# Optimization experiments

Measured on AMD Instinct MI355X. Metric: run time of the kernel, lower is better.

## Reference

```python
import jax, jax.numpy as jnp
import numpy as np

N_NODES = 100000  # size_u + size_v + size_w
N_MP = 3          # metapaths vv, uu, ww
N_EDGES = 1000000
D_IN = 64
D_OUT = 64


def setup_inputs() -> dict:
    key = jax.random.key(0)
    k1, k2, k3, k4 = jax.random.split(key, 4)
    x = jax.random.normal(k1, (N_NODES, D_IN), dtype=jnp.float32)
    # per-metapath GCNConv weight (glorot-ish scale)
    W = jax.random.normal(k2, (N_MP, D_IN, D_OUT), dtype=jnp.float32) * (1.0 / np.sqrt(D_IN))
    edge_index = jax.random.randint(k3, (N_MP, 2, N_EDGES), 0, N_NODES, dtype=jnp.int64)
    edge_weight = jax.random.uniform(k4, (N_MP, N_EDGES), dtype=jnp.float32)
    return {"x": x, "W": W, "edge_index": edge_index, "edge_weight": edge_weight}


def _gcn_conv(x, w_mat, row, col, ew, num_nodes):
    # gcn_norm without self-loops: deg[i] = sum of edge weights into i
    deg = jax.ops.segment_sum(ew, col, num_segments=num_nodes)
    dinv = jnp.where(deg > 0, jax.lax.rsqrt(jnp.where(deg > 0, deg, 1.0)), 0.0)
    norm = dinv[row] * ew * dinv[col]          # [E]
    h = x @ w_mat                               # [N, D_OUT]
    msg = h[row] * norm[:, None]                # [E, D_OUT] gather + scale
    return jax.ops.segment_sum(msg, col, num_segments=num_nodes)  # scatter-add


def reference(x, W, edge_index, edge_weight):
    num_nodes = x.shape[0]
    outs = []
    for i in range(N_MP):  # small fixed loop over structurally distinct encoders
        row = edge_index[i, 0]
        col = edge_index[i, 1]
        out = _gcn_conv(x, W[i], row, col, edge_weight[i], num_nodes)
        outs.append(jax.nn.relu(out))  # act=nn.ReLU
    return jnp.stack(outs)  # [3, N, D_OUT]; dropout omitted (eval mode)
```

## Files before the change

kernel.cpp:

```cpp
#include <hip/hip_runtime.h>

#define NNODES 100000
#define NMP 3
#define NEDGES 1000000
#define D 64
#define NTOT (NMP * NNODES)
#define BINW 1024
#define NBIN 293
#define CAPB 10944
#define T1 3072
#define OVCAP 131072

typedef __attribute__((ext_vector_type(8))) short bf16x8;
typedef __attribute__((ext_vector_type(4))) float floatx4;

__device__ __forceinline__ unsigned short f2bf(float f) {
    unsigned u = __float_as_uint(f);
    u = (u + 0x7FFFu + ((u >> 16) & 1u)) >> 16;
    return (unsigned short)u;
}
__device__ __forceinline__ float bf2f_lo(unsigned u) { return __uint_as_float(u << 16); }
__device__ __forceinline__ float bf2f_hi(unsigned u) { return __uint_as_float(u & 0xFFFF0000u); }

__global__ __launch_bounds__(512) void split_kernel(const int* __restrict__ ei,
                                                    const float* __restrict__ ew,
                                                    int* __restrict__ gcur,
                                                    int* __restrict__ ovcur,
                                                    int* __restrict__ ovf,
                                                    uint2* __restrict__ A) {
    __shared__ int hist[NBIN], binstart[NBIN], cur[NBIN], gb[NBIN];
    __shared__ int sA[512], sB[512];
    __shared__ uint2 tile[T1];
    __shared__ unsigned short tbin[T1];
    __shared__ int stotal;
    const int t = threadIdx.x;
    const int mp = blockIdx.y;
    const int e0 = blockIdx.x * T1;
    for (int i = t; i < NBIN; i += 512) { hist[i] = 0; cur[i] = 0; }
    __syncthreads();
    unsigned key[6]; float w[6]; int bn[6];
#pragma unroll
    for (int i = 0; i < 6; ++i) {
        int e = e0 + i * 512 + t;
        bn[i] = -1;
        if (e < NEDGES) {
            int r = ei[(mp * 2 + 0) * NEDGES + e];
            int c = ei[(mp * 2 + 1) * NEDGES + e];
            w[i] = ew[mp * NEDGES + e];
            int cflat = mp * NNODES + c;
            int rflat = mp * NNODES + r;
            int b = cflat >> 10;
            bn[i] = b;
            key[i] = ((unsigned)(cflat & 1023) << 19) | (unsigned)rflat;
            atomicAdd(&hist[b], 1);
        }
    }
    __syncthreads();
    int v = (t < NBIN) ? hist[t] : 0;
    sA[t] = v;
    __syncthreads();
    int* src = sA; int* dst = sB;
    for (int d = 1; d < 512; d <<= 1) {
        dst[t] = src[t] + ((t >= d) ? src[t - d] : 0);
        __syncthreads();
        int* tmp = src; src = dst; dst = tmp;
    }
    if (t < NBIN) {
        binstart[t] = src[t] - v;
        gb[t] = v ? atomicAdd(&gcur[t], v) : 0;
    }
    if (t == 511) stotal = src[511];
    __syncthreads();
#pragma unroll
    for (int i = 0; i < 6; ++i) {
        if (bn[i] >= 0) {
            int rk = atomicAdd(&cur[bn[i]], 1);
            int s = binstart[bn[i]] + rk;
            tile[s] = make_uint2(key[i], __float_as_uint(w[i]));
            tbin[s] = (unsigned short)bn[i];
        }
    }
    __syncthreads();
    int tot = stotal;
    for (int s = t; s < tot; s += 512) {
        uint2 rec = tile[s];
        int b = tbin[s];
        int pos = gb[b] + (s - binstart[b]);
        if (pos < CAPB) {
            A[(size_t)b * CAPB + pos] = rec;
        } else {
            int op = atomicAdd(ovcur, 1);
            if (op < OVCAP) {
                int cflat = (b << 10) | (int)(rec.x >> 19);
                ovf[3 * op] = cflat;
                ovf[3 * op + 1] = (int)(rec.x & 0x7FFFFu);
                ovf[3 * op + 2] = (int)rec.y;
            }
        }
    }
}

__global__ __launch_bounds__(256) void compact2_kernel(const int* __restrict__ gcur,
                                                       const uint2* __restrict__ A,
                                                       const int* __restrict__ ovcur,
                                                       const int* __restrict__ ovf,
                                                       uint2* __restrict__ C,
                                                       int2* __restrict__ nodeoff,
                                                       float* __restrict__ dinv) {
    const int bin = blockIdx.x;
    __shared__ int cnt[BINW];
    __shared__ float wsum[BINW];
    __shared__ int pos[BINW];
    __shared__ int sh[256];
    const int t = threadIdx.x;
    for (int i = t; i < BINW; i += 256) { cnt[i] = 0; wsum[i] = 0.0f; }
    __syncthreads();
    const int len = min(gcur[bin], CAPB);
    const uint2* Ab = A + (size_t)bin * CAPB;
    for (int p = t; p < len; p += 256) {
        uint2 rec = Ab[p];
        atomicAdd(&cnt[rec.x >> 19], 1);
        atomicAdd(&wsum[rec.x >> 19], __uint_as_float(rec.y));
    }
    const int ovn = min(*ovcur, OVCAP);
    for (int i = t; i < ovn; i += 256) {
        int cflat = ovf[3 * i];
        if ((cflat >> 10) == bin) {
            atomicAdd(&cnt[cflat & 1023], 1);
            atomicAdd(&wsum[cflat & 1023], __int_as_float(ovf[3 * i + 2]));
        }
    }
    __syncthreads();
    int c0 = cnt[4 * t], c1 = cnt[4 * t + 1], c2 = cnt[4 * t + 2], c3 = cnt[4 * t + 3];
    int vsum = c0 + c1 + c2 + c3;
    sh[t] = vsum;
    __syncthreads();
    for (int d = 1; d < 256; d <<= 1) {
        int add = (t >= d) ? sh[t - d] : 0;
        __syncthreads();
        sh[t] += add;
        __syncthreads();
    }
    const int base = bin * CAPB;
    const int lim = base + CAPB;
    int p0 = base + sh[t] - vsum;
    int p1 = p0 + c0, p2 = p1 + c1, p3 = p2 + c2;
    pos[4 * t] = p0; pos[4 * t + 1] = p1; pos[4 * t + 2] = p2; pos[4 * t + 3] = p3;
    int starts[4] = {p0, p1, p2, p3};
    int cs[4] = {c0, c1, c2, c3};
#pragma unroll
    for (int j = 0; j < 4; ++j) {
        int cl = 4 * t + j;
        int node = (bin << 10) + cl;
        if (node < NTOT) {
            nodeoff[node] = make_int2(starts[j], cs[j]);
            float dg = wsum[cl];
            dinv[node] = (dg > 0.0f) ? rsqrtf(dg) : 0.0f;
        }
    }
    __syncthreads();
    for (int p = t; p < len; p += 256) {
        uint2 rec = Ab[p];
        int s = atomicAdd(&pos[rec.x >> 19], 1);
        if (s < lim) C[s] = make_uint2(rec.x & 0x7FFFFu, rec.y);
    }
    for (int i = t; i < ovn; i += 256) {
        int cflat = ovf[3 * i];
        if ((cflat >> 10) == bin) {
            int s = atomicAdd(&pos[cflat & 1023], 1);
            if (s < lim) C[s] = make_uint2((unsigned)ovf[3 * i + 1], (unsigned)ovf[3 * i + 2]);
        }
    }
}

__global__ __launch_bounds__(256) void prep_w_kernel(const float* __restrict__ W,
                                                     unsigned short* __restrict__ wT) {
    int idx = blockIdx.x * 256 + threadIdx.x;
    if (idx >= NMP * D * D) return;
    int mp = idx >> 12, rem = idx & 4095;
    int k = rem >> 6, n = rem & 63;
    wT[(mp * D + n) * D + k] = f2bf(W[idx]);
}

__global__ __launch_bounds__(256) void gemm_kernel(const float* __restrict__ x,
                                                   const unsigned short* __restrict__ wT,
                                                   const float* __restrict__ dinv,
                                                   unsigned short* __restrict__ h) {
    const int wave = threadIdx.x >> 6;
    const int lane = threadIdx.x & 63;
    const int rowbase = (blockIdx.x * 4 + wave) * 16;
    if (rowbase >= NNODES) return;
    const int m = lane & 15;
    const int q = lane >> 4;
    const float4* xr = (const float4*)(x + (size_t)(rowbase + m) * D);
    bf16x8 a[2];
#pragma unroll
    for (int kc = 0; kc < 2; ++kc) {
        float4 x0 = xr[kc * 8 + q * 2];
        float4 x1 = xr[kc * 8 + q * 2 + 1];
        a[kc][0] = f2bf(x0.x); a[kc][1] = f2bf(x0.y);
        a[kc][2] = f2bf(x0.z); a[kc][3] = f2bf(x0.w);
        a[kc][4] = f2bf(x1.x); a[kc][5] = f2bf(x1.y);
        a[kc][6] = f2bf(x1.z); a[kc][7] = f2bf(x1.w);
    }
#pragma unroll
    for (int mp = 0; mp < NMP; ++mp) {
        float dv[4];
#pragma unroll
        for (int r_ = 0; r_ < 4; ++r_)
            dv[r_] = dinv[mp * NNODES + rowbase + q * 4 + r_];
#pragma unroll
        for (int nt = 0; nt < 4; ++nt) {
            int ncol = nt * 16 + m;
            const bf16x8* bp = (const bf16x8*)(wT + (size_t)(mp * D + ncol) * D);
            bf16x8 b0 = bp[q];
            bf16x8 b1 = bp[4 + q];
            floatx4 acc = {0.f, 0.f, 0.f, 0.f};
            acc = __builtin_amdgcn_mfma_f32_16x16x32_bf16(a[0], b0, acc, 0, 0, 0);
            acc = __builtin_amdgcn_mfma_f32_16x16x32_bf16(a[1], b1, acc, 0, 0, 0);
            unsigned short* hp = h + ((size_t)mp * NNODES + rowbase) * D + ncol;
#pragma unroll
            for (int r_ = 0; r_ < 4; ++r_)
                hp[(q * 4 + r_) * D] = f2bf(acc[r_] * dv[r_]);
        }
    }
}

__global__ __launch_bounds__(256) void gather_kernel(const int2* __restrict__ nodeoff,
                                                     const uint2* __restrict__ dense,
                                                     const unsigned short* __restrict__ h,
                                                     const float* __restrict__ dinv,
                                                     float* __restrict__ out) {
    int w = blockIdx.x * 4 + (threadIdx.x >> 6);
    if (w >= NTOT) return;
    int lane = threadIdx.x & 63;
    int g = lane & 7;
    int f = lane >> 3;
    int2 off = nodeoff[w];
    int start = off.x, end = off.x + off.y;
    float acc[8] = {0, 0, 0, 0, 0, 0, 0, 0};
    for (int p = start; p < end; p += 16) {
        int i0 = p + g;
        int i1 = p + 8 + g;
        uint2 pr0 = (i0 < end) ? dense[i0] : make_uint2(0u, 0u);
        uint2 pr1 = (i1 < end) ? dense[i1] : make_uint2(0u, 0u);
        uint4 hv0 = ((const uint4*)(h + (size_t)pr0.x * D))[f];
        uint4 hv1 = ((const uint4*)(h + (size_t)pr1.x * D))[f];
        float n0 = __uint_as_float(pr0.y);
        float n1 = __uint_as_float(pr1.y);
        acc[0] += n0 * bf2f_lo(hv0.x); acc[1] += n0 * bf2f_hi(hv0.x);
        acc[2] += n0 * bf2f_lo(hv0.y); acc[3] += n0 * bf2f_hi(hv0.y);
        acc[4] += n0 * bf2f_lo(hv0.z); acc[5] += n0 * bf2f_hi(hv0.z);
        acc[6] += n0 * bf2f_lo(hv0.w); acc[7] += n0 * bf2f_hi(hv0.w);
        acc[0] += n1 * bf2f_lo(hv1.x); acc[1] += n1 * bf2f_hi(hv1.x);
        acc[2] += n1 * bf2f_lo(hv1.y); acc[3] += n1 * bf2f_hi(hv1.y);
        acc[4] += n1 * bf2f_lo(hv1.z); acc[5] += n1 * bf2f_hi(hv1.z);
        acc[6] += n1 * bf2f_lo(hv1.w); acc[7] += n1 * bf2f_hi(hv1.w);
    }
#pragma unroll
    for (int j = 0; j < 8; ++j) {
        acc[j] += __shfl_xor(acc[j], 1);
        acc[j] += __shfl_xor(acc[j], 2);
        acc[j] += __shfl_xor(acc[j], 4);
    }
    int k = lane & 7;
    float b0 = (k & 1) ? acc[1] : acc[0];
    float b1 = (k & 1) ? acc[3] : acc[2];
    float b2 = (k & 1) ? acc[5] : acc[4];
    float b3 = (k & 1) ? acc[7] : acc[6];
    float c0 = (k & 2) ? b1 : b0;
    float c1 = (k & 2) ? b3 : b2;
    float v  = (k & 4) ? c1 : c0;
    out[(size_t)w * D + lane] = fmaxf(v * dinv[w], 0.0f);
}

extern "C" void kernel_launch(void* const* d_in, const int* in_sizes, int n_in,
                              void* d_out, int out_size, void* d_ws, size_t ws_size,
                              hipStream_t stream) {
    const float* x  = (const float*)d_in[0];
    const float* W  = (const float*)d_in[1];
    const int*   ei = (const int*)d_in[2];
    const float* ew = (const float*)d_in[3];
    float* out = (float*)d_out;

    char* ws = (char*)d_ws;
    uint2* A           = (uint2*)(ws + 0);
    unsigned short* h  = (unsigned short*)(ws + 0);
    uint2* C           = (uint2*)(ws + 38400000);
    int2*  nodeoff     = (int2*)(ws + 64052736);
    float* dinv        = (float*)(ws + 66452736);
    unsigned short* wT = (unsigned short*)(ws + 67652736);
    int*   gcur        = (int*)(ws + 67677312);
    int*   ovcur       = (int*)(ws + 67678484);
    int*   ovf         = (int*)(ws + 67678488);

    hipMemsetAsync(gcur, 0, 1176, stream);

    split_kernel<<<dim3((NEDGES + T1 - 1) / T1, NMP), 512, 0, stream>>>(ei, ew, gcur,
                                                                        ovcur, ovf, A);
    compact2_kernel<<<NBIN, 256, 0, stream>>>(gcur, A, ovcur, ovf, C, nodeoff, dinv);
    prep_w_kernel<<<(NMP * D * D + 255) / 256, 256, 0, stream>>>(W, wT);
    gemm_kernel<<<(NNODES / 16 + 3) / 4, 256, 0, stream>>>(x, wT, dinv, h);
    gather_kernel<<<(NTOT + 3) / 4, 256, 0, stream>>>(nodeoff, C, h, dinv, out);
}
```

Baseline: 317.5 us.

## Simplify edge binning scatter, vectorize GEMM stores, and use sub-wave gather per node

The split kernel drops its shared-memory prefix scan and staging tile and has each thread write its records straight to global bin slots through per-bin atomic cursors. This removes barriers and shared traffic but makes the global writes less coalesced. The GEMM swaps the MFMA operands so each lane holds four consecutive output columns of one row, allowing packed 8-byte bf16 stores instead of scattered 2-byte stores. The gather kernel now assigns 16 lanes per node instead of a full wave, two edges per step with float4 output stores and a single shuffle reduction. This targets wasted lanes on low-degree nodes at the cost of less memory-level parallelism per node.

```diff
diff --git a/kernel.cpp b/kernel.cpp
--- a/kernel.cpp
+++ b/kernel.cpp
@@ -28,15 +28,11 @@
                                                     int* __restrict__ ovcur,
                                                     int* __restrict__ ovf,
                                                     uint2* __restrict__ A) {
-    __shared__ int hist[NBIN], binstart[NBIN], cur[NBIN], gb[NBIN];
-    __shared__ int sA[512], sB[512];
-    __shared__ uint2 tile[T1];
-    __shared__ unsigned short tbin[T1];
-    __shared__ int stotal;
+    __shared__ int hist[NBIN], cur[NBIN];
     const int t = threadIdx.x;
     const int mp = blockIdx.y;
     const int e0 = blockIdx.x * T1;
-    for (int i = t; i < NBIN; i += 512) { hist[i] = 0; cur[i] = 0; }
+    for (int i = t; i < NBIN; i += 512) hist[i] = 0;
     __syncthreads();
     unsigned key[6]; float w[6]; int bn[6];
 #pragma unroll
@@ -56,45 +52,25 @@
         }
     }
     __syncthreads();
-    int v = (t < NBIN) ? hist[t] : 0;
-    sA[t] = v;
-    __syncthreads();
-    int* src = sA; int* dst = sB;
-    for (int d = 1; d < 512; d <<= 1) {
-        dst[t] = src[t] + ((t >= d) ? src[t - d] : 0);
-        __syncthreads();
-        int* tmp = src; src = dst; dst = tmp;
-    }
-    if (t < NBIN) {
-        binstart[t] = src[t] - v;
-        gb[t] = v ? atomicAdd(&gcur[t], v) : 0;
-    }
-    if (t == 511) stotal = src[511];
+    for (int i = t; i < NBIN; i += 512) {
+        int v = hist[i];
+        cur[i] = v ? atomicAdd(&gcur[i], v) : 0;
+    }
     __syncthreads();
 #pragma unroll
     for (int i = 0; i < 6; ++i) {
         if (bn[i] >= 0) {
-            int rk = atomicAdd(&cur[bn[i]], 1);
-            int s = binstart[bn[i]] + rk;
-            tile[s] = make_uint2(key[i], __float_as_uint(w[i]));
-            tbin[s] = (unsigned short)bn[i];
-        }
-    }
-    __syncthreads();
-    int tot = stotal;
-    for (int s = t; s < tot; s += 512) {
-        uint2 rec = tile[s];
-        int b = tbin[s];
-        int pos = gb[b] + (s - binstart[b]);
-        if (pos < CAPB) {
-            A[(size_t)b * CAPB + pos] = rec;
-        } else {
-            int op = atomicAdd(ovcur, 1);
-            if (op < OVCAP) {
-                int cflat = (b << 10) | (int)(rec.x >> 19);
-                ovf[3 * op] = cflat;
-                ovf[3 * op + 1] = (int)(rec.x & 0x7FFFFu);
-                ovf[3 * op + 2] = (int)rec.y;
+            int pos = atomicAdd(&cur[bn[i]], 1);
+            if (pos < CAPB) {
+                A[(size_t)bn[i] * CAPB + pos] = make_uint2(key[i], __float_as_uint(w[i]));
+            } else {
+                int op = atomicAdd(ovcur, 1);
+                if (op < OVCAP) {
+                    int cflat = (bn[i] << 10) | (int)(key[i] >> 19);
+                    ovf[3 * op] = cflat;
+                    ovf[3 * op + 1] = (int)(key[i] & 0x7FFFFu);
+                    ovf[3 * op + 2] = __float_as_int(w[i]);
+                }
             }
         }
     }
@@ -205,23 +181,19 @@
     }
 #pragma unroll
     for (int mp = 0; mp < NMP; ++mp) {
-        float dv[4];
-#pragma unroll
-        for (int r_ = 0; r_ < 4; ++r_)
-            dv[r_] = dinv[mp * NNODES + rowbase + q * 4 + r_];
+        float dv = dinv[mp * NNODES + rowbase + m];
 #pragma unroll
         for (int nt = 0; nt < 4; ++nt) {
-            int ncol = nt * 16 + m;
-            const bf16x8* bp = (const bf16x8*)(wT + (size_t)(mp * D + ncol) * D);
+            const bf16x8* bp = (const bf16x8*)(wT + (size_t)(mp * D + nt * 16 + m) * D);
             bf16x8 b0 = bp[q];
             bf16x8 b1 = bp[4 + q];
             floatx4 acc = {0.f, 0.f, 0.f, 0.f};
-            acc = __builtin_amdgcn_mfma_f32_16x16x32_bf16(a[0], b0, acc, 0, 0, 0);
-            acc = __builtin_amdgcn_mfma_f32_16x16x32_bf16(a[1], b1, acc, 0, 0, 0);
-            unsigned short* hp = h + ((size_t)mp * NNODES + rowbase) * D + ncol;
-#pragma unroll
-            for (int r_ = 0; r_ < 4; ++r_)
-                hp[(q * 4 + r_) * D] = f2bf(acc[r_] * dv[r_]);
+            acc = __builtin_amdgcn_mfma_f32_16x16x32_bf16(b0, a[0], acc, 0, 0, 0);
+            acc = __builtin_amdgcn_mfma_f32_16x16x32_bf16(b1, a[1], acc, 0, 0, 0);
+            unsigned v0 = (unsigned)f2bf(acc[0] * dv) | ((unsigned)f2bf(acc[1] * dv) << 16);
+            unsigned v1 = (unsigned)f2bf(acc[2] * dv) | ((unsigned)f2bf(acc[3] * dv) << 16);
+            *(uint2*)(h + ((size_t)mp * NNODES + rowbase + m) * D + nt * 16 + q * 4) =
+                make_uint2(v0, v1);
         }
     }
 }
@@ -231,47 +203,35 @@
                                                      const unsigned short* __restrict__ h,
                                                      const float* __restrict__ dinv,
                                                      float* __restrict__ out) {
-    int w = blockIdx.x * 4 + (threadIdx.x >> 6);
-    if (w >= NTOT) return;
-    int lane = threadIdx.x & 63;
-    int g = lane & 7;
-    int f = lane >> 3;
+    const int tid = threadIdx.x;
+    const int wave = tid >> 6, lane = tid & 63;
+    const int sub = lane >> 4;
+    const int g = (lane >> 3) & 1;
+    const int f = lane & 7;
+    const int w = blockIdx.x * 16 + wave * 4 + sub;
     int2 off = nodeoff[w];
     int start = off.x, end = off.x + off.y;
     float acc[8] = {0, 0, 0, 0, 0, 0, 0, 0};
-    for (int p = start; p < end; p += 16) {
-        int i0 = p + g;
-        int i1 = p + 8 + g;
-        uint2 pr0 = (i0 < end) ? dense[i0] : make_uint2(0u, 0u);
-        uint2 pr1 = (i1 < end) ? dense[i1] : make_uint2(0u, 0u);
-        uint4 hv0 = ((const uint4*)(h + (size_t)pr0.x * D))[f];
-        uint4 hv1 = ((const uint4*)(h + (size_t)pr1.x * D))[f];
-        float n0 = __uint_as_float(pr0.y);
-        float n1 = __uint_as_float(pr1.y);
-        acc[0] += n0 * bf2f_lo(hv0.x); acc[1] += n0 * bf2f_hi(hv0.x);
-        acc[2] += n0 * bf2f_lo(hv0.y); acc[3] += n0 * bf2f_hi(hv0.y);
-        acc[4] += n0 * bf2f_lo(hv0.z); acc[5] += n0 * bf2f_hi(hv0.z);
-        acc[6] += n0 * bf2f_lo(hv0.w); acc[7] += n0 * bf2f_hi(hv0.w);
-        acc[0] += n1 * bf2f_lo(hv1.x); acc[1] += n1 * bf2f_hi(hv1.x);
-        acc[2] += n1 * bf2f_lo(hv1.y); acc[3] += n1 * bf2f_hi(hv1.y);
-        acc[4] += n1 * bf2f_lo(hv1.z); acc[5] += n1 * bf2f_hi(hv1.z);
-        acc[6] += n1 * bf2f_lo(hv1.w); acc[7] += n1 * bf2f_hi(hv1.w);
-    }
-#pragma unroll
-    for (int j = 0; j < 8; ++j) {
-        acc[j] += __shfl_xor(acc[j], 1);
-        acc[j] += __shfl_xor(acc[j], 2);
-        acc[j] += __shfl_xor(acc[j], 4);
-    }
-    int k = lane & 7;
-    float b0 = (k & 1) ? acc[1] : acc[0];
-    float b1 = (k & 1) ? acc[3] : acc[2];
-    float b2 = (k & 1) ? acc[5] : acc[4];
-    float b3 = (k & 1) ? acc[7] : acc[6];
-    float c0 = (k & 2) ? b1 : b0;
-    float c1 = (k & 2) ? b3 : b2;
-    float v  = (k & 4) ? c1 : c0;
-    out[(size_t)w * D + lane] = fmaxf(v * dinv[w], 0.0f);
+    for (int p = start; p < end; p += 2) {
+        int i = p + g;
+        uint2 pr = dense[min(i, end - 1)];
+        float n0 = (i < end) ? __uint_as_float(pr.y) : 0.0f;
+        uint4 hv = ((const uint4*)(h + (size_t)pr.x * D))[f];
+        acc[0] += n0 * bf2f_lo(hv.x); acc[1] += n0 * bf2f_hi(hv.x);
+        acc[2] += n0 * bf2f_lo(hv.y); acc[3] += n0 * bf2f_hi(hv.y);
+        acc[4] += n0 * bf2f_lo(hv.z); acc[5] += n0 * bf2f_hi(hv.z);
+        acc[6] += n0 * bf2f_lo(hv.w); acc[7] += n0 * bf2f_hi(hv.w);
+    }
+#pragma unroll
+    for (int j = 0; j < 8; ++j) acc[j] += __shfl_xor(acc[j], 8);
+    float dv = dinv[w];
+    float4 o = g ? make_float4(acc[4], acc[5], acc[6], acc[7])
+                 : make_float4(acc[0], acc[1], acc[2], acc[3]);
+    o.x = fmaxf(o.x * dv, 0.0f);
+    o.y = fmaxf(o.y * dv, 0.0f);
+    o.z = fmaxf(o.z * dv, 0.0f);
+    o.w = fmaxf(o.w * dv, 0.0f);
+    ((float4*)(out + (size_t)w * D))[f * 2 + g] = o;
 }
 
 extern "C" void kernel_launch(void* const* d_in, const int* in_sizes, int n_in,
@@ -301,5 +261,5 @@
     compact2_kernel<<<NBIN, 256, 0, stream>>>(gcur, A, ovcur, ovf, C, nodeoff, dinv);
     prep_w_kernel<<<(NMP * D * D + 255) / 256, 256, 0, stream>>>(W, wT);
     gemm_kernel<<<(NNODES / 16 + 3) / 4, 256, 0, stream>>>(x, wT, dinv, h);
-    gather_kernel<<<(NTOT + 3) / 4, 256, 0, stream>>>(nodeoff, C, h, dinv, out);
-}
+    gather_kernel<<<NTOT / 16, 256, 0, stream>>>(nodeoff, C, h, dinv, out);
+}
```

Measured after the change: 292.0 us. 1.09x faster.
